# Performance work log

Hardware: AMD Instinct MI355X
Metric: run time of the kernel (lower is better)

## Reference

```python
import jax, jax.numpy as jnp
import numpy as np

B, T, MED, LAB, GLU, D = 1024, 25, 145, 1956, 16, 64
H = D // 2  # 32


def _gat(h, adj, w, a):
    # h: [B, MED, 1] drug-usage counts; in_features=1 so Wh = h * w
    Wh = h * w  # [B, MED, D]
    f1 = Wh @ a[:D]  # [B, MED]
    f2 = Wh @ a[D:]  # [B, MED]
    e = jax.nn.leaky_relu(f1[:, :, None] + f2[:, None, :], 0.2)  # [B, MED, MED]
    e = jnp.where(adj > 0, e, jnp.float32(-9e15))
    attn = jax.nn.softmax(e, axis=-1)
    return jax.nn.elu(attn @ Wh)  # [B, MED, D]


def _mha(q, k, v, wq, wk, wv, wo, nh=4):
    Bq, Lq, Dm = q.shape
    dh = Dm // nh
    qh = (q @ wq).reshape(Bq, Lq, nh, dh)
    kh = (k @ wk).reshape(Bq, k.shape[1], nh, dh)
    vh = (v @ wv).reshape(Bq, v.shape[1], nh, dh)
    s = jnp.einsum('bqhd,bkhd->bhqk', qh, kh) / np.float32(np.sqrt(dh))
    a = jax.nn.softmax(s, axis=-1)
    o = jnp.einsum('bhqk,bkhd->bqhd', a, vh).reshape(Bq, Lq, Dm)
    return o @ wo


def _gated(x, g):
    # Attn_encoder: per-position gated emphasis, preserves sequence shape
    return x * jax.nn.sigmoid(x @ g)[..., None]


def setup_inputs():
    key = jax.random.key(0)
    ks = jax.random.split(key, 40)
    n = lambda i, shape, s=0.05: (jax.random.normal(ks[i], shape, dtype=jnp.float32) * s)
    inp = {
        'lab': jax.random.normal(ks[0], (B, LAB), dtype=jnp.float32),
        'glu': jax.random.normal(ks[1], (B, T, GLU), dtype=jnp.float32),
        'time_feat': jax.random.uniform(ks[2], (B, T, GLU), dtype=jnp.float32),
        'med': jax.random.uniform(ks[3], (B, T, MED), dtype=jnp.float32),
        'ehr_adj': (jax.random.uniform(ks[4], (MED, MED)) > 0.9).astype(jnp.float32),
        'ddi_adj': (jax.random.uniform(ks[5], (MED, MED)) > 0.9).astype(jnp.float32),
        'time_adj': (jax.random.uniform(ks[6], (MED, MED)) > 0.9).astype(jnp.float32),
        'sll_w1': n(7, (LAB, D)), 'sll_b1': n(8, (D,)),
        'sll_w2': n(9, (D, H)), 'sll_b2': n(10, (H,)),
        'glu_w': n(11, (2 * GLU, H)), 'glu_b': n(12, (H,)), 'glu_gate': n(13, (H,)),
        'med_w': n(14, (MED, D)), 'med_b': n(15, (D,)), 'med_gate': n(16, (D,)),
        'gat_ehr_w': n(17, (D,)), 'gat_ehr_a': n(18, (2 * D,)),
        'gat_time_w': n(19, (D,)), 'gat_time_a': n(20, (2 * D,)),
        'gat_ddi_w': n(21, (D,)), 'gat_ddi_a': n(22, (2 * D,)),
        'ga_wq': n(23, (D, D)), 'ga_wk': n(24, (D, D)), 'ga_wv': n(25, (D, D)), 'ga_wo': n(26, (D, D)),
        'm1_wq': n(27, (D, D)), 'm1_wk': n(28, (D, D)), 'm1_wv': n(29, (D, D)), 'm1_wo': n(30, (D, D)),
        'm2_wq': n(31, (D, D)), 'm2_wk': n(32, (D, D)), 'm2_wv': n(33, (D, D)), 'm2_wo': n(34, (D, D)),
        'out_w1': n(35, (MED * D, MED * D // 8), 0.01), 'out_b1': n(36, (MED * D // 8,)),
        'out_w2': n(37, (MED * D // 8, MED)), 'out_b2': n(38, (MED,)),
    }
    return inp


def reference(lab, glu, time_feat, med, ehr_adj, ddi_adj, time_adj,
              sll_w1, sll_b1, sll_w2, sll_b2,
              glu_w, glu_b, glu_gate, med_w, med_b, med_gate,
              gat_ehr_w, gat_ehr_a, gat_time_w, gat_time_a, gat_ddi_w, gat_ddi_a,
              ga_wq, ga_wk, ga_wv, ga_wo,
              m1_wq, m1_wk, m1_wv, m1_wo,
              m2_wq, m2_wk, m2_wv, m2_wo,
              out_w1, out_b1, out_w2, out_b2):
    relu = jax.nn.relu
    medb = (med > 0.9).astype(med.dtype)  # multi-hot medication history
    # static_ll, repeated over visits
    static = relu(relu(lab @ sll_w1 + sll_b1) @ sll_w2 + sll_b2)  # [B, H]
    static_seq = jnp.broadcast_to(static[:, None, :], (B, T, H))
    # per-patient drug usage counts over past visits
    h = jnp.sum(medb[:, :-1], axis=1)[..., None]  # [B, MED, 1]
    g_ehr = _gat(h, ehr_adj, gat_ehr_w, gat_ehr_a)
    g_time = _gat(h, time_adj, gat_time_w, gat_time_a)
    g_ddi = _gat(h, ddi_adj, gat_ddi_w, gat_ddi_a)
    all_graph = jnp.concatenate([g_ehr, g_time, g_ddi], axis=1)  # [B, 3*MED, D]
    dm = _mha(all_graph, all_graph, all_graph, ga_wq, ga_wk, ga_wv, ga_wo)
    drug_mem = dm.reshape(B, 3, MED, D).mean(axis=1)  # [B, MED, D]
    # medication / glucose encoders
    med_rep = _gated(medb[:, :-1] @ med_w + med_b, med_gate)  # [B, T-1, D]
    glu_in = jnp.concatenate([glu, time_feat], axis=-1)  # [B, T, 2*GLU]
    glu_rep = _gated(jnp.tanh(glu_in @ glu_w + glu_b), glu_gate)  # [B, T, H]
    patient = jnp.concatenate([glu_rep, static_seq], axis=-1)  # [B, T, D]
    # m1: query = med history, keys/values = patient visits
    E_en = _mha(med_rep, patient, patient, m1_wq, m1_wk, m1_wv, m1_wo)  # [B, T-1, D]
    e0 = E_en[:, :1]  # [B, 1, D]
    # m2: query = drug memory, keys/values = encoded state
    E_de = _mha(drug_mem, e0, e0, m2_wq, m2_wk, m2_wv, m2_wo)  # [B, MED, D]
    final = E_de.reshape(B, MED * D)
    hid = relu(relu(final) @ out_w1 + out_b1)
    return hid @ out_w2 + out_b2  # [B, MED]
```

## Files before the change

kernel.cpp:

```cpp
#include <hip/hip_runtime.h>
#include <math.h>

#define B_   1024
#define T_   25
#define MED_ 145
#define LAB_ 1956
#define GLU_ 16
#define D_   64
#define H_   32
#define HID_ 1160
#define KC_  978

__global__ __launch_bounds__(512) void k_static_a(
    const float* __restrict__ lab, const float* __restrict__ w1,
    float* __restrict__ part) {
  const int b0 = blockIdx.x * 8;
  const int kc = blockIdx.y;
  const int k0 = kc * KC_;
  const int tid = threadIdx.x;
  __shared__ float2 lab_s2[8][KC_ / 2];
  for (int e = tid; e < 8 * (KC_ / 2); e += 512) {
    int r = e / (KC_ / 2), i = e - r * (KC_ / 2);
    lab_s2[r][i] = ((const float2*)(lab + (size_t)(b0 + r) * LAB_ + k0))[i];
  }
  __syncthreads();
  const float* lab_f = (const float*)lab_s2;
  const int col = tid & 63;
  const int slice = tid >> 6;
  float acc[8] = {0.f, 0.f, 0.f, 0.f, 0.f, 0.f, 0.f, 0.f};
  #pragma unroll 2
  for (int k = slice; k < KC_; k += 8) {
    float w = w1[(size_t)(k0 + k) * D_ + col];
    #pragma unroll
    for (int r = 0; r < 8; ++r) acc[r] = fmaf(lab_f[r * KC_ + k], w, acc[r]);
  }
  __syncthreads();
  __shared__ float red[8][8][64];
  #pragma unroll
  for (int r = 0; r < 8; ++r) red[r][slice][col] = acc[r];
  __syncthreads();
  {
    int r = tid >> 6, d = tid & 63;
    float v = 0.f;
    #pragma unroll
    for (int s2 = 0; s2 < 8; ++s2) v += red[r][s2][d];
    part[(size_t)kc * B_ * D_ + (size_t)(b0 + r) * D_ + d] = v;
  }
}

__global__ __launch_bounds__(256) void k_static_b(
    const float* __restrict__ part, const float* __restrict__ b1,
    const float* __restrict__ w2, const float* __restrict__ b2,
    float* __restrict__ st) {
  const int b0 = blockIdx.x * 4;
  const int tid = threadIdx.x;
  __shared__ float t1[4][64];
  {
    int r = tid >> 6, d = tid & 63;
    size_t o = (size_t)(b0 + r) * D_ + d;
    float v = part[o] + part[(size_t)B_ * D_ + o] + b1[d];
    t1[r][d] = fmaxf(v, 0.f);
  }
  __syncthreads();
  if (tid < 128) {
    int r = tid >> 5, j = tid & 31;
    float s = b2[j];
    #pragma unroll 8
    for (int d = 0; d < D_; ++d) s = fmaf(t1[r][d], w2[d * H_ + j], s);
    st[(size_t)(b0 + r) * H_ + j] = fmaxf(s, 0.f);
  }
}

__global__ __launch_bounds__(256) void k_w1c(const float* __restrict__ w1,
                                             float* __restrict__ w1c) {
  const int idx = blockIdx.x * 256 + threadIdx.x;
  const int mq = blockIdx.y;
  const int m0 = (mq * MED_) >> 2, m1 = ((mq + 1) * MED_) >> 2;
  const float* p = w1 + idx + (size_t)m0 * D_ * HID_;
  float s = 0.f;
  #pragma unroll 8
  for (int m = m0; m < m1; ++m) {
    s += *p;
    p += (size_t)D_ * HID_;
  }
  atomicAdd(&w1c[idx], s);
}

__global__ __launch_bounds__(256) void k_perb(
    const float* __restrict__ glu, const float* __restrict__ tf,
    const float* __restrict__ med, const float* __restrict__ st,
    const float* __restrict__ glu_w, const float* __restrict__ glu_b,
    const float* __restrict__ glu_gate, const float* __restrict__ med_w,
    const float* __restrict__ med_b, const float* __restrict__ med_gate,
    const float* __restrict__ wq, const float* __restrict__ wk,
    const float* __restrict__ wv, const float* __restrict__ wo,
    const float* __restrict__ m2wv, const float* __restrict__ m2wo,
    float* __restrict__ rr) {
  const int b = blockIdx.x;
  const int tid = threadIdx.x;
  const int d = tid & 63;
  const int s4 = tid >> 6;
  __shared__ float xin_s[T_][2 * GLU_];
  __shared__ float y_s[T_][H_];
  __shared__ float gate_s[T_];
  __shared__ float medrow_s[MED_];
  __shared__ float pat_s[28][D_];
  __shared__ float q0_s[D_];
  __shared__ float kh_s[T_][D_];
  __shared__ float vh_s[T_][D_];
  __shared__ float sc_s[4][T_];
  __shared__ float at_s[4][T_];
  __shared__ float o_s[D_];
  __shared__ float vec_s[D_];
  __shared__ float red4[4][D_];

  for (int e = tid; e < T_ * GLU_; e += 256) {
    int t = e >> 4, i = e & 15;
    xin_s[t][i] = glu[((size_t)b * T_ + t) * GLU_ + i];
    xin_s[t][GLU_ + i] = tf[((size_t)b * T_ + t) * GLU_ + i];
  }
  if (tid < MED_) medrow_s[tid] = med[(size_t)b * T_ * MED_ + tid];
  __syncthreads();

  for (int e = tid; e < T_ * H_; e += 256) {
    int t = e >> 5, j = e & 31;
    float s = glu_b[j];
    #pragma unroll 8
    for (int i = 0; i < 2 * GLU_; ++i) s = fmaf(xin_s[t][i], glu_w[i * H_ + j], s);
    y_s[t][j] = tanhf(s);
  }
  __syncthreads();

  if (tid < 8 * T_) {
    int t = tid >> 3, sl = tid & 7;
    float s = 0.f;
    #pragma unroll
    for (int i = 0; i < 4; ++i) {
      int j = sl * 4 + i;
      s = fmaf(y_s[t][j], glu_gate[j], s);
    }
    s += __shfl_xor(s, 1);
    s += __shfl_xor(s, 2);
    s += __shfl_xor(s, 4);
    if (sl == 0) gate_s[t] = 1.f / (1.f + __expf(-s));
  }
  {
    float x = 0.f;
    for (int m = s4; m < MED_; m += 4)
      if (medrow_s[m] > 0.9f) x += med_w[m * D_ + d];
    red4[s4][d] = x;
  }
  __syncthreads();

  if (tid < D_) {
    float x = med_b[tid] + red4[0][tid] + red4[1][tid] + red4[2][tid] + red4[3][tid];
    float v = x * med_gate[tid];
    #pragma unroll
    for (int off = 32; off > 0; off >>= 1) v += __shfl_xor(v, off);
    q0_s[tid] = x * (1.f / (1.f + __expf(-v)));
  }
  for (int e = tid; e < 28 * H_; e += 256) {
    int t = e >> 5, j = e & 31;
    if (t < T_) {
      pat_s[t][j] = y_s[t][j] * gate_s[t];
      pat_s[t][H_ + j] = st[(size_t)b * H_ + j];
    } else {
      pat_s[t][j] = 0.f;
      pat_s[t][H_ + j] = 0.f;
    }
  }
  __syncthreads();

  {
    float aK[7] = {0.f, 0.f, 0.f, 0.f, 0.f, 0.f, 0.f};
    float aV[7] = {0.f, 0.f, 0.f, 0.f, 0.f, 0.f, 0.f};
    #pragma unroll 4
    for (int j = 0; j < D_; ++j) {
      float wkj = wk[j * D_ + d];
      float wvj = wv[j * D_ + d];
      #pragma unroll
      for (int i = 0; i < 7; ++i) {
        float p = pat_s[s4 + 4 * i][j];
        aK[i] = fmaf(p, wkj, aK[i]);
        aV[i] = fmaf(p, wvj, aV[i]);
      }
    }
    #pragma unroll
    for (int i = 0; i < 7; ++i) {
      int t = s4 + 4 * i;
      if (t < T_) { kh_s[t][d] = aK[i]; vh_s[t][d] = aV[i]; }
    }
  }
  {
    float qp = 0.f;
    #pragma unroll
    for (int i = 0; i < 16; ++i) {
      int j = s4 * 16 + i;
      qp = fmaf(q0_s[j], wq[j * D_ + d], qp);
    }
    red4[s4][d] = qp;
  }
  __syncthreads();
  if (tid < D_) vec_s[tid] = red4[0][tid] + red4[1][tid] + red4[2][tid] + red4[3][tid];
  __syncthreads();

  if (tid < 4 * T_) {
    int h = tid / T_, t = tid - h * T_;
    float s = 0.f;
    #pragma unroll
    for (int i = 0; i < 16; ++i) s = fmaf(vec_s[h * 16 + i], kh_s[t][h * 16 + i], s);
    sc_s[h][t] = s * 0.25f;
  }
  __syncthreads();
  if (tid < 4) {
    float m = -1e30f;
    for (int t = 0; t < T_; ++t) m = fmaxf(m, sc_s[tid][t]);
    float sum = 0.f;
    for (int t = 0; t < T_; ++t) {
      float e = __expf(sc_s[tid][t] - m);
      at_s[tid][t] = e;
      sum += e;
    }
    float inv = 1.f / sum;
    for (int t = 0; t < T_; ++t) at_s[tid][t] *= inv;
  }
  __syncthreads();
  if (tid < D_) {
    int h = tid >> 4;
    float s = 0.f;
    #pragma unroll
    for (int t = 0; t < T_; ++t) s = fmaf(at_s[h][t], vh_s[t][tid], s);
    o_s[tid] = s;
  }
  __syncthreads();
  {
    float p = 0.f;
    #pragma unroll
    for (int i = 0; i < 16; ++i) {
      int j = s4 * 16 + i;
      p = fmaf(o_s[j], wo[j * D_ + d], p);
    }
    red4[s4][d] = p;
  }
  __syncthreads();
  if (tid < D_) vec_s[tid] = red4[0][tid] + red4[1][tid] + red4[2][tid] + red4[3][tid];
  __syncthreads();
  {
    float p = 0.f;
    #pragma unroll
    for (int i = 0; i < 16; ++i) {
      int j = s4 * 16 + i;
      p = fmaf(vec_s[j], m2wv[j * D_ + d], p);
    }
    red4[s4][d] = p;
  }
  __syncthreads();
  if (tid < D_) o_s[tid] = red4[0][tid] + red4[1][tid] + red4[2][tid] + red4[3][tid];
  __syncthreads();
  {
    float p = 0.f;
    #pragma unroll
    for (int i = 0; i < 16; ++i) {
      int j = s4 * 16 + i;
      p = fmaf(o_s[j], m2wo[j * D_ + d], p);
    }
    red4[s4][d] = p;
  }
  __syncthreads();
  if (tid < D_) {
    float v = red4[0][tid] + red4[1][tid] + red4[2][tid] + red4[3][tid];
    rr[(size_t)b * D_ + tid] = fmaxf(v, 0.f);
  }
}

__global__ __launch_bounds__(640) void k_final(
    const float* __restrict__ rr, const float* __restrict__ w1c,
    const float* __restrict__ b1, const float* __restrict__ w2,
    const float* __restrict__ b2, float* __restrict__ out) {
  const int tid = threadIdx.x;
  const int b0 = blockIdx.x * 16;
  const int jq = blockIdx.y;
  const int j0 = jq * 290;
  __shared__ float rr_s[16][D_];
  __shared__ float hid_s[16][292];
  for (int e = tid; e < 16 * D_; e += 640)
    ((float*)rr_s)[e] = rr[(size_t)b0 * D_ + e];
  __syncthreads();
  if (tid < 580) {
    int jj = tid % 290, rh = tid / 290;
    const float* wp = w1c + (size_t)(j0 + jj);
    float bb = b1[j0 + jj];
    float acc[8] = {0.f, 0.f, 0.f, 0.f, 0.f, 0.f, 0.f, 0.f};
    #pragma unroll 4
    for (int d4 = 0; d4 < 16; ++d4) {
      float w0 = wp[(size_t)(4 * d4 + 0) * HID_];
      float w1v = wp[(size_t)(4 * d4 + 1) * HID_];
      float w2v = wp[(size_t)(4 * d4 + 2) * HID_];
      float w3v = wp[(size_t)(4 * d4 + 3) * HID_];
      #pragma unroll
      for (int r8 = 0; r8 < 8; ++r8) {
        float4 rv = *(const float4*)&rr_s[rh * 8 + r8][4 * d4];
        acc[r8] += rv.x * w0 + rv.y * w1v + rv.z * w2v + rv.w * w3v;
      }
    }
    #pragma unroll
    for (int r8 = 0; r8 < 8; ++r8)
      hid_s[rh * 8 + r8][jj] = fmaxf(acc[r8] + bb, 0.f);
  }
  __syncthreads();
  if (tid < 580) {
    int n = tid % MED_, rg = tid / MED_;
    const float* w2p = w2 + (size_t)j0 * MED_ + n;
    float s0 = 0.f, s1 = 0.f, s2 = 0.f, s3 = 0.f;
    #pragma unroll 4
    for (int jv = 0; jv < 72; ++jv) {
      float wa = w2p[(size_t)(4 * jv + 0) * MED_];
      float wb = w2p[(size_t)(4 * jv + 1) * MED_];
      float wc = w2p[(size_t)(4 * jv + 2) * MED_];
      float wd = w2p[(size_t)(4 * jv + 3) * MED_];
      float4 h0 = *(const float4*)&hid_s[rg * 4 + 0][4 * jv];
      float4 h1 = *(const float4*)&hid_s[rg * 4 + 1][4 * jv];
      float4 h2 = *(const float4*)&hid_s[rg * 4 + 2][4 * jv];
      float4 h3 = *(const float4*)&hid_s[rg * 4 + 3][4 * jv];
      s0 += h0.x * wa + h0.y * wb + h0.z * wc + h0.w * wd;
      s1 += h1.x * wa + h1.y * wb + h1.z * wc + h1.w * wd;
      s2 += h2.x * wa + h2.y * wb + h2.z * wc + h2.w * wd;
      s3 += h3.x * wa + h3.y * wb + h3.z * wc + h3.w * wd;
    }
    {
      float wa = w2p[(size_t)288 * MED_];
      float wb = w2p[(size_t)289 * MED_];
      s0 += hid_s[rg * 4 + 0][288] * wa + hid_s[rg * 4 + 0][289] * wb;
      s1 += hid_s[rg * 4 + 1][288] * wa + hid_s[rg * 4 + 1][289] * wb;
      s2 += hid_s[rg * 4 + 2][288] * wa + hid_s[rg * 4 + 2][289] * wb;
      s3 += hid_s[rg * 4 + 3][288] * wa + hid_s[rg * 4 + 3][289] * wb;
    }
    float bias = (jq == 0) ? b2[n] : 0.f;
    atomicAdd(&out[(size_t)(b0 + rg * 4 + 0) * MED_ + n], s0 + bias);
    atomicAdd(&out[(size_t)(b0 + rg * 4 + 1) * MED_ + n], s1 + bias);
    atomicAdd(&out[(size_t)(b0 + rg * 4 + 2) * MED_ + n], s2 + bias);
    atomicAdd(&out[(size_t)(b0 + rg * 4 + 3) * MED_ + n], s3 + bias);
  }
}

extern "C" void kernel_launch(void* const* d_in, const int* in_sizes, int n_in,
                              void* d_out, int out_size, void* d_ws, size_t ws_size,
                              hipStream_t stream) {
  (void)in_sizes; (void)n_in; (void)out_size; (void)ws_size;
  const float* lab      = (const float*)d_in[0];
  const float* glu      = (const float*)d_in[1];
  const float* tf       = (const float*)d_in[2];
  const float* med      = (const float*)d_in[3];
  const float* sll_w1   = (const float*)d_in[7];
  const float* sll_b1   = (const float*)d_in[8];
  const float* sll_w2   = (const float*)d_in[9];
  const float* sll_b2   = (const float*)d_in[10];
  const float* glu_w    = (const float*)d_in[11];
  const float* glu_b    = (const float*)d_in[12];
  const float* glu_gate = (const float*)d_in[13];
  const float* med_w    = (const float*)d_in[14];
  const float* med_b    = (const float*)d_in[15];
  const float* med_gate = (const float*)d_in[16];
  const float* m1_wq    = (const float*)d_in[27];
  const float* m1_wk    = (const float*)d_in[28];
  const float* m1_wv    = (const float*)d_in[29];
  const float* m1_wo    = (const float*)d_in[30];
  const float* m2_wv    = (const float*)d_in[33];
  const float* m2_wo    = (const float*)d_in[34];
  const float* out_w1   = (const float*)d_in[35];
  const float* out_b1   = (const float*)d_in[36];
  const float* out_w2   = (const float*)d_in[37];
  const float* out_b2   = (const float*)d_in[38];
  float* out = (float*)d_out;

  float* ws   = (float*)d_ws;
  float* st   = ws;
  float* rr   = st + B_ * H_;
  float* w1c  = rr + B_ * D_;
  float* part = w1c + D_ * HID_;

  hipLaunchKernelGGL(k_static_a, dim3(B_ / 8, 2), dim3(512), 0, stream,
                     lab, sll_w1, part);
  hipLaunchKernelGGL(k_static_b, dim3(B_ / 4), dim3(256), 0, stream,
                     part, sll_b1, sll_w2, sll_b2, st);
  hipMemsetAsync(w1c, 0, (size_t)D_ * HID_ * sizeof(float), stream);
  hipMemsetAsync(out, 0, (size_t)B_ * MED_ * sizeof(float), stream);
  hipLaunchKernelGGL(k_w1c, dim3((D_ * HID_) / 256, 4), dim3(256), 0, stream,
                     out_w1, w1c);
  hipLaunchKernelGGL(k_perb, dim3(B_), dim3(256), 0, stream,
                     glu, tf, med, st, glu_w, glu_b, glu_gate,
                     med_w, med_b, med_gate,
                     m1_wq, m1_wk, m1_wv, m1_wo, m2_wv, m2_wo, rr);
  hipLaunchKernelGGL(k_final, dim3(B_ / 16, 4), dim3(640), 0, stream,
                     rr, w1c, out_b1, out_w2, out_b2, out);
}
```

Measured before the change: 244.7 us.

## Fuse preprocessing kernels, fold weight chain, replace atomics with partial-sum combine

Merges the static-lab GEMM, the out_w1 column reduction and a new precomputation of the wo·m2_wv·m2_wo weight product into one multi-role kernel. The static MLP second layer moves into the per-batch kernel, and the two trailing matvecs there collapse into one with the folded matrix. The softmax is rewritten with wave shuffles. Final-layer atomics and memsets are replaced by four partial buffers plus a combine kernel. This cuts launches, atomics and serial sync steps, at the cost of an extra kernel and an extra pass over the output.

```diff
diff --git a/kernel.cpp b/kernel.cpp
--- a/kernel.cpp
+++ b/kernel.cpp
@@ -10,91 +10,87 @@
 #define H_   32
 #define HID_ 1160
 #define KC_  978
-
-__global__ __launch_bounds__(512) void k_static_a(
-    const float* __restrict__ lab, const float* __restrict__ w1,
-    float* __restrict__ part) {
-  const int b0 = blockIdx.x * 8;
-  const int kc = blockIdx.y;
-  const int k0 = kc * KC_;
+#define OUTN_ (B_ * MED_)
+
+__global__ __launch_bounds__(512) void k_pre(
+    const float* __restrict__ lab, const float* __restrict__ sw1,
+    const float* __restrict__ out_w1,
+    const float* __restrict__ wo, const float* __restrict__ m2wv,
+    const float* __restrict__ m2wo,
+    float* __restrict__ part, float* __restrict__ w1c, float* __restrict__ W3) {
+  __shared__ float smem[11920];
   const int tid = threadIdx.x;
-  __shared__ float2 lab_s2[8][KC_ / 2];
-  for (int e = tid; e < 8 * (KC_ / 2); e += 512) {
-    int r = e / (KC_ / 2), i = e - r * (KC_ / 2);
-    lab_s2[r][i] = ((const float2*)(lab + (size_t)(b0 + r) * LAB_ + k0))[i];
-  }
-  __syncthreads();
-  const float* lab_f = (const float*)lab_s2;
-  const int col = tid & 63;
-  const int slice = tid >> 6;
-  float acc[8] = {0.f, 0.f, 0.f, 0.f, 0.f, 0.f, 0.f, 0.f};
-  #pragma unroll 2
-  for (int k = slice; k < KC_; k += 8) {
-    float w = w1[(size_t)(k0 + k) * D_ + col];
-    #pragma unroll
-    for (int r = 0; r < 8; ++r) acc[r] = fmaf(lab_f[r * KC_ + k], w, acc[r]);
-  }
-  __syncthreads();
-  __shared__ float red[8][8][64];
-  #pragma unroll
-  for (int r = 0; r < 8; ++r) red[r][slice][col] = acc[r];
-  __syncthreads();
-  {
-    int r = tid >> 6, d = tid & 63;
-    float v = 0.f;
-    #pragma unroll
-    for (int s2 = 0; s2 < 8; ++s2) v += red[r][s2][d];
-    part[(size_t)kc * B_ * D_ + (size_t)(b0 + r) * D_ + d] = v;
-  }
-}
-
-__global__ __launch_bounds__(256) void k_static_b(
-    const float* __restrict__ part, const float* __restrict__ b1,
-    const float* __restrict__ w2, const float* __restrict__ b2,
-    float* __restrict__ st) {
-  const int b0 = blockIdx.x * 4;
-  const int tid = threadIdx.x;
-  __shared__ float t1[4][64];
-  {
-    int r = tid >> 6, d = tid & 63;
-    size_t o = (size_t)(b0 + r) * D_ + d;
-    float v = part[o] + part[(size_t)B_ * D_ + o] + b1[d];
-    t1[r][d] = fmaxf(v, 0.f);
-  }
-  __syncthreads();
-  if (tid < 128) {
-    int r = tid >> 5, j = tid & 31;
-    float s = b2[j];
+  const int bid = blockIdx.x;
+  if (bid < 256) {
+    const int b0 = (bid >> 1) * 8;
+    const int kc = bid & 1;
+    const int k0 = kc * KC_;
+    float* lab_f = smem;
+    float* red   = smem + 7824;
+    for (int e = tid; e < 8 * 489; e += 512) {
+      int r = e / 489, i = e - r * 489;
+      float2 v = ((const float2*)(lab + (size_t)(b0 + r) * LAB_ + k0))[i];
+      lab_f[r * 978 + 2 * i] = v.x;
+      lab_f[r * 978 + 2 * i + 1] = v.y;
+    }
+    __syncthreads();
+    const int col = tid & 63;
+    const int slice = tid >> 6;
+    float acc[8] = {0.f, 0.f, 0.f, 0.f, 0.f, 0.f, 0.f, 0.f};
+    #pragma unroll 2
+    for (int k = slice; k < KC_; k += 8) {
+      float w = sw1[(size_t)(k0 + k) * D_ + col];
+      #pragma unroll
+      for (int r = 0; r < 8; ++r) acc[r] = fmaf(lab_f[r * 978 + k], w, acc[r]);
+    }
+    __syncthreads();
+    #pragma unroll
+    for (int r = 0; r < 8; ++r) red[(r * 8 + slice) * 64 + col] = acc[r];
+    __syncthreads();
+    {
+      int r = tid >> 6, d = tid & 63;
+      float v = 0.f;
+      #pragma unroll
+      for (int s2 = 0; s2 < 8; ++s2) v += red[(r * 8 + s2) * 64 + d];
+      part[(size_t)kc * B_ * D_ + (size_t)(b0 + r) * D_ + d] = v;
+    }
+  } else if (bid < 401) {
+    const int idx = (bid - 256) * 512 + tid;
+    const float* p = out_w1 + idx;
+    float s = 0.f;
     #pragma unroll 8
-    for (int d = 0; d < D_; ++d) s = fmaf(t1[r][d], w2[d * H_ + j], s);
-    st[(size_t)(b0 + r) * H_ + j] = fmaxf(s, 0.f);
-  }
-}
-
-__global__ __launch_bounds__(256) void k_w1c(const float* __restrict__ w1,
-                                             float* __restrict__ w1c) {
-  const int idx = blockIdx.x * 256 + threadIdx.x;
-  const int mq = blockIdx.y;
-  const int m0 = (mq * MED_) >> 2, m1 = ((mq + 1) * MED_) >> 2;
-  const float* p = w1 + idx + (size_t)m0 * D_ * HID_;
-  float s = 0.f;
-  #pragma unroll 8
-  for (int m = m0; m < m1; ++m) {
-    s += *p;
-    p += (size_t)D_ * HID_;
-  }
-  atomicAdd(&w1c[idx], s);
+    for (int m = 0; m < MED_; ++m) s += p[(size_t)m * D_ * HID_];
+    w1c[idx] = s;
+  } else {
+    float* tmp = smem;
+    for (int e = tid; e < 4096; e += 512) {
+      int i = e >> 6, j = e & 63;
+      float s = 0.f;
+      #pragma unroll 8
+      for (int k = 0; k < 64; ++k) s = fmaf(wo[i * 64 + k], m2wv[k * 64 + j], s);
+      tmp[e] = s;
+    }
+    __syncthreads();
+    for (int e = tid; e < 4096; e += 512) {
+      int i = e >> 6, j = e & 63;
+      float s = 0.f;
+      #pragma unroll 8
+      for (int k = 0; k < 64; ++k) s = fmaf(tmp[i * 64 + k], m2wo[k * 64 + j], s);
+      W3[e] = s;
+    }
+  }
 }
 
 __global__ __launch_bounds__(256) void k_perb(
     const float* __restrict__ glu, const float* __restrict__ tf,
-    const float* __restrict__ med, const float* __restrict__ st,
+    const float* __restrict__ med, const float* __restrict__ part,
+    const float* __restrict__ sb1, const float* __restrict__ sw2,
+    const float* __restrict__ sb2,
     const float* __restrict__ glu_w, const float* __restrict__ glu_b,
     const float* __restrict__ glu_gate, const float* __restrict__ med_w,
     const float* __restrict__ med_b, const float* __restrict__ med_gate,
     const float* __restrict__ wq, const float* __restrict__ wk,
-    const float* __restrict__ wv, const float* __restrict__ wo,
-    const float* __restrict__ m2wv, const float* __restrict__ m2wo,
+    const float* __restrict__ wv, const float* __restrict__ W3,
     float* __restrict__ rr) {
   const int b = blockIdx.x;
   const int tid = threadIdx.x;
@@ -103,12 +99,13 @@
   __shared__ float xin_s[T_][2 * GLU_];
   __shared__ float y_s[T_][H_];
   __shared__ float gate_s[T_];
-  __shared__ float medrow_s[MED_];
+  __shared__ float medrow_s[160];
+  __shared__ float t1_s[D_];
+  __shared__ float st_s[H_];
   __shared__ float pat_s[28][D_];
   __shared__ float q0_s[D_];
   __shared__ float kh_s[T_][D_];
   __shared__ float vh_s[T_][D_];
-  __shared__ float sc_s[4][T_];
   __shared__ float at_s[4][T_];
   __shared__ float o_s[D_];
   __shared__ float vec_s[D_];
@@ -120,6 +117,11 @@
     xin_s[t][GLU_ + i] = tf[((size_t)b * T_ + t) * GLU_ + i];
   }
   if (tid < MED_) medrow_s[tid] = med[(size_t)b * T_ * MED_ + tid];
+  if (tid >= 192) {
+    int dd = tid - 192;
+    size_t o = (size_t)b * D_ + dd;
+    t1_s[dd] = fmaxf(part[o] + part[(size_t)B_ * D_ + o] + sb1[dd], 0.f);
+  }
   __syncthreads();
 
   for (int e = tid; e < T_ * H_; e += 256) {
@@ -129,27 +131,34 @@
     for (int i = 0; i < 2 * GLU_; ++i) s = fmaf(xin_s[t][i], glu_w[i * H_ + j], s);
     y_s[t][j] = tanhf(s);
   }
-  __syncthreads();
-
-  if (tid < 8 * T_) {
-    int t = tid >> 3, sl = tid & 7;
-    float s = 0.f;
-    #pragma unroll
-    for (int i = 0; i < 4; ++i) {
-      int j = sl * 4 + i;
-      s = fmaf(y_s[t][j], glu_gate[j], s);
-    }
-    s += __shfl_xor(s, 1);
-    s += __shfl_xor(s, 2);
-    s += __shfl_xor(s, 4);
-    if (sl == 0) gate_s[t] = 1.f / (1.f + __expf(-s));
-  }
+  if (tid >= 224) {
+    int j = tid - 224;
+    float s = sb2[j];
+    #pragma unroll 8
+    for (int dd = 0; dd < D_; ++dd) s = fmaf(t1_s[dd], sw2[dd * H_ + j], s);
+    st_s[j] = fmaxf(s, 0.f);
+  }
+  __syncthreads();
+
   {
     float x = 0.f;
     for (int m = s4; m < MED_; m += 4)
       if (medrow_s[m] > 0.9f) x += med_w[m * D_ + d];
     red4[s4][d] = x;
   }
+  if (tid < 8 * T_) {
+    int t = tid >> 3, sl = tid & 7;
+    float s = 0.f;
+    #pragma unroll
+    for (int i = 0; i < 4; ++i) {
+      int j = sl * 4 + i;
+      s = fmaf(y_s[t][j], glu_gate[j], s);
+    }
+    s += __shfl_xor(s, 1);
+    s += __shfl_xor(s, 2);
+    s += __shfl_xor(s, 4);
+    if (sl == 0) gate_s[t] = 1.f / (1.f + __expf(-s));
+  }
   __syncthreads();
 
   if (tid < D_) {
@@ -163,7 +172,7 @@
     int t = e >> 5, j = e & 31;
     if (t < T_) {
       pat_s[t][j] = y_s[t][j] * gate_s[t];
-      pat_s[t][H_ + j] = st[(size_t)b * H_ + j];
+      pat_s[t][H_ + j] = st_s[j];
     } else {
       pat_s[t][j] = 0.f;
       pat_s[t][H_ + j] = 0.f;
@@ -201,30 +210,31 @@
     red4[s4][d] = qp;
   }
   __syncthreads();
+
   if (tid < D_) vec_s[tid] = red4[0][tid] + red4[1][tid] + red4[2][tid] + red4[3][tid];
   __syncthreads();
 
-  if (tid < 4 * T_) {
-    int h = tid / T_, t = tid - h * T_;
-    float s = 0.f;
-    #pragma unroll
-    for (int i = 0; i < 16; ++i) s = fmaf(vec_s[h * 16 + i], kh_s[t][h * 16 + i], s);
-    sc_s[h][t] = s * 0.25f;
-  }
-  __syncthreads();
-  if (tid < 4) {
-    float m = -1e30f;
-    for (int t = 0; t < T_; ++t) m = fmaxf(m, sc_s[tid][t]);
-    float sum = 0.f;
-    for (int t = 0; t < T_; ++t) {
-      float e = __expf(sc_s[tid][t] - m);
-      at_s[tid][t] = e;
-      sum += e;
-    }
-    float inv = 1.f / sum;
-    for (int t = 0; t < T_; ++t) at_s[tid][t] *= inv;
-  }
-  __syncthreads();
+  if (tid < 128) {
+    int h = tid >> 5, t = tid & 31;
+    bool valid = t < T_;
+    float sc = -3.4e38f;
+    if (valid) {
+      float a = 0.f;
+      #pragma unroll
+      for (int i = 0; i < 16; ++i) a = fmaf(vec_s[h * 16 + i], kh_s[t][h * 16 + i], a);
+      sc = a * 0.25f;
+    }
+    float m = sc;
+    #pragma unroll
+    for (int off = 16; off > 0; off >>= 1) m = fmaxf(m, __shfl_xor(m, off, 32));
+    float e = valid ? __expf(sc - m) : 0.f;
+    float sum = e;
+    #pragma unroll
+    for (int off = 16; off > 0; off >>= 1) sum += __shfl_xor(sum, off, 32);
+    if (valid) at_s[h][t] = e / sum;
+  }
+  __syncthreads();
+
   if (tid < D_) {
     int h = tid >> 4;
     float s = 0.f;
@@ -233,40 +243,18 @@
     o_s[tid] = s;
   }
   __syncthreads();
+
   {
     float p = 0.f;
     #pragma unroll
     for (int i = 0; i < 16; ++i) {
       int j = s4 * 16 + i;
-      p = fmaf(o_s[j], wo[j * D_ + d], p);
+      p = fmaf(o_s[j], W3[j * D_ + d], p);
     }
     red4[s4][d] = p;
   }
   __syncthreads();
-  if (tid < D_) vec_s[tid] = red4[0][tid] + red4[1][tid] + red4[2][tid] + red4[3][tid];
-  __syncthreads();
-  {
-    float p = 0.f;
-    #pragma unroll
-    for (int i = 0; i < 16; ++i) {
-      int j = s4 * 16 + i;
-      p = fmaf(vec_s[j], m2wv[j * D_ + d], p);
-    }
-    red4[s4][d] = p;
-  }
-  __syncthreads();
-  if (tid < D_) o_s[tid] = red4[0][tid] + red4[1][tid] + red4[2][tid] + red4[3][tid];
-  __syncthreads();
-  {
-    float p = 0.f;
-    #pragma unroll
-    for (int i = 0; i < 16; ++i) {
-      int j = s4 * 16 + i;
-      p = fmaf(o_s[j], m2wo[j * D_ + d], p);
-    }
-    red4[s4][d] = p;
-  }
-  __syncthreads();
+
   if (tid < D_) {
     float v = red4[0][tid] + red4[1][tid] + red4[2][tid] + red4[3][tid];
     rr[(size_t)b * D_ + tid] = fmaxf(v, 0.f);
@@ -276,7 +264,7 @@
 __global__ __launch_bounds__(640) void k_final(
     const float* __restrict__ rr, const float* __restrict__ w1c,
     const float* __restrict__ b1, const float* __restrict__ w2,
-    const float* __restrict__ b2, float* __restrict__ out) {
+    float* __restrict__ p4) {
   const int tid = threadIdx.x;
   const int b0 = blockIdx.x * 16;
   const int jq = blockIdx.y;
@@ -335,12 +323,21 @@
       s2 += hid_s[rg * 4 + 2][288] * wa + hid_s[rg * 4 + 2][289] * wb;
       s3 += hid_s[rg * 4 + 3][288] * wa + hid_s[rg * 4 + 3][289] * wb;
     }
-    float bias = (jq == 0) ? b2[n] : 0.f;
-    atomicAdd(&out[(size_t)(b0 + rg * 4 + 0) * MED_ + n], s0 + bias);
-    atomicAdd(&out[(size_t)(b0 + rg * 4 + 1) * MED_ + n], s1 + bias);
-    atomicAdd(&out[(size_t)(b0 + rg * 4 + 2) * MED_ + n], s2 + bias);
-    atomicAdd(&out[(size_t)(b0 + rg * 4 + 3) * MED_ + n], s3 + bias);
-  }
+    float* dst = p4 + (size_t)jq * OUTN_;
+    dst[(size_t)(b0 + rg * 4 + 0) * MED_ + n] = s0;
+    dst[(size_t)(b0 + rg * 4 + 1) * MED_ + n] = s1;
+    dst[(size_t)(b0 + rg * 4 + 2) * MED_ + n] = s2;
+    dst[(size_t)(b0 + rg * 4 + 3) * MED_ + n] = s3;
+  }
+}
+
+__global__ __launch_bounds__(256) void k_combine(
+    const float* __restrict__ p4, const float* __restrict__ b2,
+    float* __restrict__ out) {
+  int idx = blockIdx.x * 256 + threadIdx.x;
+  int n = idx - (idx / MED_) * MED_;
+  out[idx] = p4[idx] + p4[OUTN_ + idx] + p4[2 * OUTN_ + idx] +
+             p4[3 * OUTN_ + idx] + b2[n];
 }
 
 extern "C" void kernel_launch(void* const* d_in, const int* in_sizes, int n_in,
@@ -374,23 +371,20 @@
   float* out = (float*)d_out;
 
   float* ws   = (float*)d_ws;
-  float* st   = ws;
-  float* rr   = st + B_ * H_;
-  float* w1c  = rr + B_ * D_;
-  float* part = w1c + D_ * HID_;
-
-  hipLaunchKernelGGL(k_static_a, dim3(B_ / 8, 2), dim3(512), 0, stream,
-                     lab, sll_w1, part);
-  hipLaunchKernelGGL(k_static_b, dim3(B_ / 4), dim3(256), 0, stream,
-                     part, sll_b1, sll_w2, sll_b2, st);
-  hipMemsetAsync(w1c, 0, (size_t)D_ * HID_ * sizeof(float), stream);
-  hipMemsetAsync(out, 0, (size_t)B_ * MED_ * sizeof(float), stream);
-  hipLaunchKernelGGL(k_w1c, dim3((D_ * HID_) / 256, 4), dim3(256), 0, stream,
-                     out_w1, w1c);
+  float* part = ws;
+  float* w1c  = part + 2 * B_ * D_;
+  float* rr   = w1c + D_ * HID_;
+  float* W3   = rr + B_ * D_;
+  float* p4   = W3 + D_ * D_;
+
+  hipLaunchKernelGGL(k_pre, dim3(402), dim3(512), 0, stream,
+                     lab, sll_w1, out_w1, m1_wo, m2_wv, m2_wo, part, w1c, W3);
   hipLaunchKernelGGL(k_perb, dim3(B_), dim3(256), 0, stream,
-                     glu, tf, med, st, glu_w, glu_b, glu_gate,
-                     med_w, med_b, med_gate,
-                     m1_wq, m1_wk, m1_wv, m1_wo, m2_wv, m2_wo, rr);
+                     glu, tf, med, part, sll_b1, sll_w2, sll_b2,
+                     glu_w, glu_b, glu_gate, med_w, med_b, med_gate,
+                     m1_wq, m1_wk, m1_wv, W3, rr);
   hipLaunchKernelGGL(k_final, dim3(B_ / 16, 4), dim3(640), 0, stream,
-                     rr, w1c, out_b1, out_w2, out_b2, out);
-}
+                     rr, w1c, out_b1, out_w2, p4);
+  hipLaunchKernelGGL(k_combine, dim3(OUTN_ / 256), dim3(256), 0, stream,
+                     p4, out_b2, out);
+}
```

After: 249.4 us. No clear change (+1.9%).
